# Optimization experiments

Hardware: AMD Instinct MI355X
Metric: run time of the kernel (lower is better)

The kernel has to match this reference:

```python
import jax, jax.numpy as jnp
import numpy as np
import math

B, T, C, H, LC, DFF = 2, 1024, 1024, 16, 256, 4096
EPS = 1e-6


def _ln(x):
    # LayerNorm without affine (elementwise_affine=False under AdaLN), eps=1e-6
    m = jnp.mean(x, -1, keepdims=True)
    v = jnp.mean((x - m) ** 2, -1, keepdims=True)
    return (x - m) * jax.lax.rsqrt(v + EPS)


def _heads(t):
    b, l, c = t.shape
    return t.reshape(b, l, H, c // H).transpose(0, 2, 1, 3)  # (b,H,l,dh)


def _unheads(t):
    b, h, l, d = t.shape
    return t.transpose(0, 2, 1, 3).reshape(b, l, h * d)


def setup_inputs():
    key = jax.random.key(0)
    ks = jax.random.split(key, 16)
    s = 0.02
    p = lambda k, sh: jax.random.normal(k, sh, jnp.float32) * s
    x_star = jax.random.normal(ks[0], (B, T, C), jnp.float32)
    x_hat = jax.random.normal(ks[1], (B, T, C), jnp.float32)
    c = jax.random.normal(ks[2], (B, LC, C), jnp.float32)
    chunk = jnp.sort(jax.random.randint(ks[3], (B, T), 0, 32), axis=1)
    m_star = chunk[:, :, None] > chunk[:, None, :]   # attend to strictly earlier chunks
    m_hat = chunk[:, :, None] == chunk[:, None, :]   # attend within same chunk
    dep_mask = jax.random.bernoulli(ks[4], 0.98, (B, T, T)) | jnp.eye(T, dtype=bool)[None]
    return dict(
        x_star=x_star, x_hat=x_hat, c=c,
        m_star=m_star, m_hat=m_hat, dep_mask=dep_mask,
        ncond_g=jnp.ones((C,), jnp.float32), ncond_b=jnp.zeros((C,), jnp.float32),
        Wq=p(ks[5], (C, C)), bq=jnp.zeros((C,), jnp.float32),
        Wkv=p(ks[6], (C, 2 * C)), bkv=jnp.zeros((2 * C,), jnp.float32),
        Wco=p(ks[7], (C, C)), bco=jnp.zeros((C,), jnp.float32),
        Wada=p(ks[8], (C, 6 * C)), bada=jnp.zeros((6 * C,), jnp.float32),
        Wqkv=p(ks[9], (C, 3 * C)), bqkv=jnp.zeros((3 * C,), jnp.float32),
        Wo=p(ks[10], (C, C)), bo=jnp.zeros((C,), jnp.float32),
        W1=p(ks[11], (C, DFF)), b1=jnp.zeros((DFF,), jnp.float32),
        W2=p(ks[12], (DFF, C)), b2=jnp.zeros((C,), jnp.float32),
    )


def _cross_attn(x, c, Wq, bq, Wkv, bkv, Wco, bco):
    q = _heads(x @ Wq + bq)
    k, v = jnp.split(c @ Wkv + bkv, 2, -1)
    k, v = _heads(k), _heads(v)
    att = jnp.einsum('bhtd,bhsd->bhts', q, k) / math.sqrt(C // H)
    y = jnp.einsum('bhts,bhsd->bhtd', jax.nn.softmax(att, -1), v)
    return _unheads(y) @ Wco + bco


def _interleave(xs, xh, m_star, m_hat, dep, Wqkv, bqkv, Wo, bo):
    # Attention.forward_interleave (eval: dropout identity)
    NEG = -jnp.inf
    sc = 1.0 / math.sqrt(C // H)
    qkv = lambda x: [_heads(t) for t in jnp.split(x @ Wqkv + bqkv, 3, -1)]
    qs, ks, vs = qkv(xs)
    qh, kh, vh = qkv(xh)
    blk_star = (~m_star)[:, None]     # True -> block
    blk_hat = (~m_hat)[:, None]
    blk_dep = (~dep)[:, None]
    causal = jnp.triu(jnp.ones((T, T), bool), 1)[None, None]
    # star stream: causal + dependency mask
    att_star = jnp.einsum('bhtd,bhsd->bhts', qs, ks) * sc
    att_star = jnp.where(blk_dep, NEG, att_star)
    p_star = jax.nn.softmax(jnp.where(causal, NEG, att_star), -1)
    y_star = _unheads(jnp.einsum('bhts,bhsd->bhtd', p_star, vs)) @ Wo + bo
    # hat stream: merge logits (q_hat vs k_star on earlier chunks, q_hat vs k_hat within chunk)
    a1 = jnp.where(blk_star, NEG, jnp.einsum('bhtd,bhsd->bhts', qh, ks) * sc)
    a2 = jnp.where(blk_hat, NEG, jnp.einsum('bhtd,bhsd->bhts', qh, kh) * sc)
    merged = jnp.where(jnp.isinf(a2), a1, a2)
    merged = jnp.where(blk_dep, NEG, merged)
    p_hat = jax.nn.softmax(merged, -1)
    y_hat = jnp.einsum('bhts,bhsd->bhtd', jnp.where(blk_star, 0.0, p_hat), vs) \
          + jnp.einsum('bhts,bhsd->bhtd', jnp.where(blk_hat, 0.0, p_hat), vh)
    y_hat = _unheads(y_hat) @ Wo + bo
    return y_star, y_hat


def reference(x_star, x_hat, c, m_star, m_hat, dep_mask,
              ncond_g, ncond_b, Wq, bq, Wkv, bkv, Wco, bco, Wada, bada,
              Wqkv, bqkv, Wo, bo, W1, b1, W2, b2):
    mod = lambda x, sh, scale: x * (1 + scale) + sh
    mlp = lambda x: jax.nn.gelu(x @ W1 + b1, approximate=True) @ W2 + b2
    ca = lambda x: _cross_attn(_ln(x) * ncond_g + ncond_b, c, Wq, bq, Wkv, bkv, Wco, bco)
    ada = lambda t: jnp.split(jax.nn.silu(t) @ Wada + bada, 6, -1)
    gs = ada(ca(x_star))
    gh = ada(ca(x_hat))
    ms = mod(_ln(x_star), gs[0], gs[1])
    mh = mod(_ln(x_hat), gh[0], gh[1])
    ys, yh = _interleave(ms, mh, m_star, m_hat, dep_mask, Wqkv, bqkv, Wo, bo)
    x_star = x_star + gs[2] * ys
    x_hat = x_hat + gh[2] * yh
    x_star = x_star + gs[5] * mlp(mod(_ln(x_star), gs[3], gs[4]))
    x_hat = x_hat + gh[5] * mlp(mod(_ln(x_hat), gh[3], gh[4]))
    return x_star, x_hat
```

## Files before the change

### kernel.cpp

```cpp
#include <hip/hip_runtime.h>
#include <hip/hip_bf16.h>
#include <stdint.h>

#define DEVI __device__ __forceinline__

typedef __bf16 bf16x8 __attribute__((ext_vector_type(8)));
typedef float f32x4 __attribute__((ext_vector_type(4)));
typedef unsigned short us;
typedef unsigned long long ull;

DEVI float b2f(us u) { union { unsigned int i; float f; } v; v.i = ((unsigned int)u) << 16; return v.f; }
DEVI us f2b(float f) {
  union { unsigned int i; float f; } v; v.f = f;
  unsigned int r = (v.i + 0x7fffu + ((v.i >> 16) & 1u)) >> 16;
  return (us)r;
}

#define NEGINF (-__builtin_inff())

DEVI void gl2lds16(const us* g, us* l) {
  __builtin_amdgcn_global_load_lds(
      (const __attribute__((address_space(1))) unsigned int*)g,
      (__attribute__((address_space(3))) unsigned int*)l, 16, 0, 0);
}

__global__ __launch_bounds__(256) void detect_flags(
    const unsigned int* __restrict__ xw, const unsigned int* __restrict__ mw,
    int* __restrict__ flags) {
  const int t = threadIdx.x;
  int cnt = 0, big = 0;
  for (int i = t; i < 4096; i += 256) {
    unsigned int w = xw[i];
    us lo = (us)(w & 0xffffu);
    float a = fabsf(b2f(lo));
    cnt += ((lo == 0) || (a >= 1e-8f && a <= 256.f)) ? 1 : 0;
    big |= (mw[i] > 1u) ? 1 : 0;
  }
  for (int o = 32; o; o >>= 1) { cnt += __shfl_down(cnt, o); big |= __shfl_down(big, o); }
  __shared__ int sc[4], sb[4];
  if ((t & 63) == 0) { sc[t >> 6] = cnt; sb[t >> 6] = big; }
  __syncthreads();
  if (t == 0) {
    flags[0] = (sc[0] + sc[1] + sc[2] + sc[3] < 2048) ? 1 : 0;
    flags[1] = (sb[0] | sb[1] | sb[2] | sb[3]);
  }
}

__global__ __launch_bounds__(256) void cvt_bf16(
    const void* __restrict__ src, us* __restrict__ dst, int n,
    const int* __restrict__ flags) {
  const int f32mode = flags[0];
  int idx = (blockIdx.x * 256 + threadIdx.x) * 4;
  if (idx >= n) return;
  if (f32mode) {
    const float* s = (const float*)src;
    float4 v = *(const float4*)(s + idx);
    dst[idx] = f2b(v.x); dst[idx + 1] = f2b(v.y);
    dst[idx + 2] = f2b(v.z); dst[idx + 3] = f2b(v.w);
  } else {
    *(uint2*)(dst + idx) = *(const uint2*)((const us*)src + idx);
  }
}

struct P10 { const void* p[10]; };
__global__ __launch_bounds__(256) void cvt_small(P10 ps, us* __restrict__ dst,
                                                 const int* __restrict__ flags) {
  const int offs[11] = {0, 1024, 2048, 3072, 5120, 6144, 12288, 15360, 16384, 20480, 21504};
  int idx = blockIdx.x * 256 + threadIdx.x;
  if (idx >= 21504) return;
  int seg = 0;
#pragma unroll
  for (int i = 1; i < 10; ++i) seg += (idx >= offs[i]) ? 1 : 0;
  int local = idx - offs[seg];
  float v = flags[0] ? ((const float*)ps.p[seg])[local]
                     : b2f(((const us*)ps.p[seg])[local]);
  dst[idx] = f2b(v);
}

__global__ __launch_bounds__(256) void transpose_cvt64(
    const void* __restrict__ W, us* __restrict__ WT, int K, int N,
    const int* __restrict__ flags) {
  __shared__ __attribute__((aligned(16))) us tile[64 * 72];
  const int f32m = flags[0];
  const int k0 = blockIdx.x * 64, n0 = blockIdx.y * 64;
  const int t = threadIdx.x;
  const int row = t >> 2, colb = (t & 3) * 16;
  const int sw = ((row >> 4) & 3) << 4;
  us tmp[16];
  if (f32m) {
    const float* src = (const float*)W + (size_t)(k0 + row) * N + n0 + colb;
#pragma unroll
    for (int i = 0; i < 16; i += 4) {
      float4 v = *(const float4*)(src + i);
      tmp[i] = f2b(v.x); tmp[i + 1] = f2b(v.y); tmp[i + 2] = f2b(v.z); tmp[i + 3] = f2b(v.w);
    }
  } else {
    const us* src = (const us*)W + (size_t)(k0 + row) * N + n0 + colb;
    *(uint4*)tmp = *(const uint4*)src;
    *(uint4*)(tmp + 8) = *(const uint4*)(src + 8);
  }
  *(uint4*)&tile[row * 72 + (colb ^ sw)] = *(uint4*)tmp;
  *(uint4*)&tile[row * 72 + (colb ^ sw) + 8] = *(uint4*)(tmp + 8);
  __syncthreads();
  const int orow = t >> 2, ocolb = (t & 3) * 16;
  const int pc = (orow & 15) | ((orow & 48) ^ (ocolb & 48));
  us out[16];
#pragma unroll
  for (int i = 0; i < 16; ++i) out[i] = tile[(ocolb + i) * 72 + pc];
  us* dst = WT + (size_t)(n0 + orow) * K + k0 + ocolb;
  *(uint4*)dst = *(uint4*)out;
  *(uint4*)(dst + 8) = *(uint4*)(out + 8);
}

struct P3 { const void* p[3]; };
__global__ __launch_bounds__(256) void pack_mask3(P3 ms, ull* __restrict__ bits,
                                                  const int* __restrict__ flags) {
  const int bytemode = flags[1];
  const void* m = ms.p[blockIdx.y];
  ull* out = bits + (size_t)blockIdx.y * 32768;
  int wv = blockIdx.x * 4 + (threadIdx.x >> 6);
  int lane = threadIdx.x & 63;
  for (int w = 0; w < 16; ++w) {
    int v;
    if (bytemode) v = ((const unsigned char*)m)[(size_t)wv * 1024 + w * 64 + lane];
    else          v = ((const int*)m)[(size_t)wv * 1024 + w * 64 + lane];
    ull b = __ballot(v != 0);
    if (lane == 0) out[(size_t)wv * 16 + w] = b;
  }
}

__global__ __launch_bounds__(256) void hat_blockflags(
    const ull* __restrict__ starb, const ull* __restrict__ hatb, int* __restrict__ bf) {
  const int bt = blockIdx.x;
  const int b = bt >> 4, tt = bt & 15;
  const int t = threadIdx.x, wv = t >> 6, lane = t & 63;
  const int t0 = tt * 64;
  for (int k = 0; k < 4; ++k) {
    int ck = wv * 4 + k;
    ull sw = starb[(size_t)(b * 1024 + t0 + lane) * 16 + ck];
    ull hw = hatb[(size_t)(b * 1024 + t0 + lane) * 16 + ck];
    int f = (__ballot(sw != 0ull) ? 1 : 0) | (__ballot(hw != 0ull) ? 2 : 0);
    if (lane == 0) bf[bt * 16 + ck] = f;
  }
}

__global__ __launch_bounds__(256) void vtrans(
    const us* __restrict__ src, us* __restrict__ dst,
    int T, int stride, int colBase, int rowOff) {
  __shared__ __attribute__((aligned(16))) us tile[64][65];
  const int bh = blockIdx.y, b = bh >> 4, h = bh & 15;
  const int t0 = blockIdx.x * 64;
  const int t = threadIdx.x;
#pragma unroll
  for (int it = 0; it < 2; ++it) {
    int idx = it * 256 + t; int r = idx >> 3, c8 = (idx & 7) * 8;
    uint4 d4 = *(const uint4*)(src + (size_t)(rowOff + b * T + t0 + r) * stride + colBase + h * 64 + c8);
    const us* e = (const us*)&d4;
#pragma unroll
    for (int i = 0; i < 8; ++i) tile[r][c8 + i] = e[i];
  }
  __syncthreads();
#pragma unroll
  for (int it = 0; it < 2; ++it) {
    int idx = it * 256 + t; int d = idx >> 3, c8 = (idx & 7) * 8;
    us tmp[8];
#pragma unroll
    for (int i = 0; i < 8; ++i) tmp[i] = tile[c8 + i][d];
    *(uint4*)(dst + ((size_t)(bh * 64 + d)) * T + t0 + c8) = *(const uint4*)tmp;
  }
}

__global__ __launch_bounds__(256) void ln_affine(
    const void* __restrict__ xs, const void* __restrict__ xh,
    const us* __restrict__ gw, const us* __restrict__ bw,
    us* __restrict__ lnx, us* __restrict__ xn, const int* __restrict__ flags) {
  const int f32m = flags[0];
  const int row = blockIdx.x;
  const void* xp = (row < 2048) ? xs : xh;
  const size_t base = (size_t)(row & 2047) * 1024;
  const int t = threadIdx.x;
  float v[4]; float s = 0.f, ss = 0.f;
#pragma unroll
  for (int i = 0; i < 4; ++i) {
    size_t idx = base + i * 256 + t;
    float x = f32m ? ((const float*)xp)[idx] : b2f(((const us*)xp)[idx]);
    v[i] = x; s += x; ss += x * x;
  }
  for (int o = 32; o; o >>= 1) { s += __shfl_down(s, o); ss += __shfl_down(ss, o); }
  __shared__ float red[2][4];
  const int wv = t >> 6, lane = t & 63;
  if (lane == 0) { red[0][wv] = s; red[1][wv] = ss; }
  __syncthreads();
  s = red[0][0] + red[0][1] + red[0][2] + red[0][3];
  ss = red[1][0] + red[1][1] + red[1][2] + red[1][3];
  const float mean = s * (1.f / 1024.f);
  const float var = fmaxf(ss * (1.f / 1024.f) - mean * mean, 0.f);
  const float rstd = rsqrtf(var + 1e-6f);
  const size_t ro = (size_t)row * 1024;
#pragma unroll
  for (int i = 0; i < 4; ++i) {
    int c = i * 256 + t;
    float n = (v[i] - mean) * rstd;
    lnx[ro + c] = f2b(n);
    xn[ro + c] = f2b(n * b2f(gw[c]) + b2f(bw[c]));
  }
}

__global__ __launch_bounds__(256) void mod_ms(
    const us* __restrict__ lnx, const us* __restrict__ gada, us* __restrict__ ms) {
  const size_t idx = ((size_t)blockIdx.x * 256 + threadIdx.x) * 4;
  const int row = (int)(idx >> 10), c = (int)(idx & 1023);
  const size_t gb = (size_t)row * 6144;
#pragma unroll
  for (int i = 0; i < 4; ++i) {
    float sh = b2f(gada[gb + c + i]);
    float sc = b2f(gada[gb + 1024 + c + i]);
    ms[idx + i] = f2b(b2f(lnx[idx + i]) * (1.f + sc) + sh);
  }
}

__global__ __launch_bounds__(256) void ln_mod(
    const float* __restrict__ x1, const us* __restrict__ gada, us* __restrict__ m2) {
  const int row = blockIdx.x;
  const float* xp = x1 + (size_t)row * 1024;
  const int t = threadIdx.x;
  float v[4]; float s = 0.f, ss = 0.f;
#pragma unroll
  for (int i = 0; i < 4; ++i) { float x = xp[i * 256 + t]; v[i] = x; s += x; ss += x * x; }
  for (int o = 32; o; o >>= 1) { s += __shfl_down(s, o); ss += __shfl_down(ss, o); }
  __shared__ float red[2][4];
  const int wv = t >> 6, lane = t & 63;
  if (lane == 0) { red[0][wv] = s; red[1][wv] = ss; }
  __syncthreads();
  s = red[0][0] + red[0][1] + red[0][2] + red[0][3];
  ss = red[1][0] + red[1][1] + red[1][2] + red[1][3];
  const float mean = s * (1.f / 1024.f);
  const float var = fmaxf(ss * (1.f / 1024.f) - mean * mean, 0.f);
  const float rstd = rsqrtf(var + 1e-6f);
  const size_t gb = (size_t)row * 6144;
#pragma unroll
  for (int i = 0; i < 4; ++i) {
    int c = i * 256 + t;
    float n = (v[i] - mean) * rstd;
    float sh = b2f(gada[gb + 3072 + c]);
    float sc = b2f(gada[gb + 4096 + c]);
    m2[(size_t)row * 1024 + c] = f2b(n * (1.f + sc) + sh);
  }
}

enum { EPI_BF16 = 0, EPI_SILU, EPI_GELU, EPI_GATE_XRES, EPI_GATE_OUT };

template <int EPI>
DEVI void gemm_epi(float v, int gmr, int gn, int N, void* out,
                   const us* gate, const void* res0, const void* res1,
                   const int* oflags) {
  const size_t oi = (size_t)gmr * N + gn;
  if constexpr (EPI == EPI_BF16) {
    ((us*)out)[oi] = f2b(v);
  } else if constexpr (EPI == EPI_SILU) {
    ((us*)out)[oi] = f2b(v / (1.f + __expf(-v)));
  } else if constexpr (EPI == EPI_GELU) {
    float u = 0.7978845608028654f * (v + 0.044715f * v * v * v);
    float th = 1.f - 2.f / (__expf(2.f * u) + 1.f);
    ((us*)out)[oi] = f2b(0.5f * v * (1.f + th));
  } else if constexpr (EPI == EPI_GATE_XRES) {
    float g = b2f(gate[(size_t)gmr * 6144 + gn]);
    const void* xr = (gmr < 2048) ? res0 : res1;
    size_t xi = (size_t)(gmr & 2047) * 1024 + gn;
    float x = oflags[0] ? ((const float*)xr)[xi] : b2f(((const us*)xr)[xi]);
    ((float*)out)[oi] = x + g * v;
  } else {
    float g = b2f(gate[(size_t)gmr * 6144 + gn]);
    float x = ((const float*)res0)[oi];
    float r2 = x + g * v;
    if (oflags[0]) ((float*)out)[oi] = r2;
    else ((us*)out)[oi] = f2b(r2);
  }
}

template <int EPI>
__global__ __launch_bounds__(256) void gemm_bt(
    const us* __restrict__ A, const us* __restrict__ BT,
    const us* __restrict__ bias, void* __restrict__ out,
    int M, int N, int K,
    const us* __restrict__ gate,
    const void* __restrict__ res0, const void* __restrict__ res1,
    const int* __restrict__ oflags) {
  __shared__ __attribute__((aligned(16))) us As[2][128 * 32];
  __shared__ __attribute__((aligned(16))) us Bs[2][128 * 32];
  const int m0 = blockIdx.x * 128, n0 = blockIdx.y * 128;
  const int t = threadIdx.x;
  const int wave = t >> 6, lane = t & 63;
  const int wm = (wave >> 1) * 64, wn = (wave & 1) * 64;
  const int l16 = lane & 15, quad = lane >> 4;
  f32x4 acc[4][4] = {};

  const int lr = lane >> 2, lc = (lane & 3) * 8;
  const us* gA = A + (size_t)(m0 + wave * 32 + lr) * K + lc;
  const us* gB = BT + (size_t)(n0 + wave * 32 + lr) * K + lc;
  const int wo = wave * 1024;

  gl2lds16(gA, &As[0][wo]);
  gl2lds16(gA + (size_t)16 * K, &As[0][wo + 512]);
  gl2lds16(gB, &Bs[0][wo]);
  gl2lds16(gB + (size_t)16 * K, &Bs[0][wo + 512]);

  int cur = 0;
  for (int k0 = 0; k0 < K; k0 += 32) {
    __syncthreads();
    const int nk = k0 + 32;
    if (nk < K) {
      us* pA = &As[cur ^ 1][wo];
      us* pB = &Bs[cur ^ 1][wo];
      gl2lds16(gA + nk, pA);
      gl2lds16(gA + (size_t)16 * K + nk, pA + 512);
      gl2lds16(gB + nk, pB);
      gl2lds16(gB + (size_t)16 * K + nk, pB + 512);
    }
    bf16x8 af[4], bfv[4];
#pragma unroll
    for (int i = 0; i < 4; ++i) af[i] = *(const bf16x8*)(const void*)&As[cur][(wm + i * 16 + l16) * 32 + quad * 8];
#pragma unroll
    for (int j = 0; j < 4; ++j) bfv[j] = *(const bf16x8*)(const void*)&Bs[cur][(wn + j * 16 + l16) * 32 + quad * 8];
#pragma unroll
    for (int i = 0; i < 4; ++i)
#pragma unroll
      for (int j = 0; j < 4; ++j)
        acc[i][j] = __builtin_amdgcn_mfma_f32_16x16x32_bf16(af[i], bfv[j], acc[i][j], 0, 0, 0);
    cur ^= 1;
  }

#pragma unroll
  for (int i = 0; i < 4; ++i) {
    const int gm = m0 + wm + i * 16 + quad * 4;
#pragma unroll
    for (int j = 0; j < 4; ++j) {
      const int gn = n0 + wn + j * 16 + l16;
      const float bv = b2f(bias[gn]);
#pragma unroll
      for (int r = 0; r < 4; ++r)
        gemm_epi<EPI>(acc[i][j][r] + bv, gm + r, gn, N, out, gate, res0, res1, oflags);
    }
  }
}

template <int EPI>
__global__ __launch_bounds__(256) void gemm_bt64(
    const us* __restrict__ A, const us* __restrict__ BT,
    const us* __restrict__ bias, void* __restrict__ out,
    int M, int N, int K,
    const us* __restrict__ gate,
    const void* __restrict__ res0, const void* __restrict__ res1,
    const int* __restrict__ oflags) {
  __shared__ __attribute__((aligned(16))) us As[2][128 * 32];
  __shared__ __attribute__((aligned(16))) us Bs[2][64 * 32];
  const int m0 = blockIdx.x * 128, n0 = blockIdx.y * 64;
  const int t = threadIdx.x;
  const int wave = t >> 6, lane = t & 63;
  const int wm = (wave >> 1) * 64, wn = (wave & 1) * 32;
  const int l16 = lane & 15, quad = lane >> 4;
  f32x4 acc[4][2] = {};

  const int lr = lane >> 2, lc = (lane & 3) * 8;
  const us* gA = A + (size_t)(m0 + wave * 32 + lr) * K + lc;
  const us* gB = BT + (size_t)(n0 + wave * 16 + lr) * K + lc;
  const int woA = wave * 1024, woB = wave * 512;

  gl2lds16(gA, &As[0][woA]);
  gl2lds16(gA + (size_t)16 * K, &As[0][woA + 512]);
  gl2lds16(gB, &Bs[0][woB]);

  int cur = 0;
  for (int k0 = 0; k0 < K; k0 += 32) {
    __syncthreads();
    const int nk = k0 + 32;
    if (nk < K) {
      us* pA = &As[cur ^ 1][woA];
      gl2lds16(gA + nk, pA);
      gl2lds16(gA + (size_t)16 * K + nk, pA + 512);
      gl2lds16(gB + nk, &Bs[cur ^ 1][woB]);
    }
    bf16x8 af[4], bfv[2];
#pragma unroll
    for (int i = 0; i < 4; ++i) af[i] = *(const bf16x8*)(const void*)&As[cur][(wm + i * 16 + l16) * 32 + quad * 8];
#pragma unroll
    for (int j = 0; j < 2; ++j) bfv[j] = *(const bf16x8*)(const void*)&Bs[cur][(wn + j * 16 + l16) * 32 + quad * 8];
#pragma unroll
    for (int i = 0; i < 4; ++i)
#pragma unroll
      for (int j = 0; j < 2; ++j)
        acc[i][j] = __builtin_amdgcn_mfma_f32_16x16x32_bf16(af[i], bfv[j], acc[i][j], 0, 0, 0);
    cur ^= 1;
  }

#pragma unroll
  for (int i = 0; i < 4; ++i) {
    const int gm = m0 + wm + i * 16 + quad * 4;
#pragma unroll
    for (int j = 0; j < 2; ++j) {
      const int gn = n0 + wn + j * 16 + l16;
      const float bv = b2f(bias[gn]);
#pragma unroll
      for (int r = 0; r < 4; ++r)
        gemm_epi<EPI>(acc[i][j][r] + bv, gm + r, gn, N, out, gate, res0, res1, oflags);
    }
  }
}

struct AttnState { float m[4], l[4]; f32x4 o[4]; };

DEVI void st_init(AttnState& s) {
#pragma unroll
  for (int r = 0; r < 4; ++r) { s.m[r] = NEGINF; s.l[r] = 0.f; s.o[r] = f32x4{}; }
}

DEVI void stage64(us* __restrict__ dst, const us* __restrict__ src,
                  int strideUs, int t) {
#pragma unroll
  for (int it = 0; it < 2; ++it) {
    const int id = it * 256 + t;
    const int row = id >> 3, c8 = (id & 7) * 8;
    *(uint4*)&dst[row * 72 + c8] = *(const uint4*)(src + (size_t)row * strideUs + c8);
  }
}

template <bool MASKED>
DEVI void attn_round(const us* __restrict__ Kb, const us* __restrict__ Vb,
                     us* __restrict__ Pb, const ull* mrow,
                     bf16x8 aq0, bf16x8 aq1, AttnState& st,
                     int wv, int l16, int quad) {
  f32x4 s[4];
#pragma unroll
  for (int j = 0; j < 4; ++j) {
    const int row = j * 16 + l16;
    bf16x8 bk0 = *(const bf16x8*)(const void*)&Kb[row * 72 + quad * 8];
    bf16x8 bk1 = *(const bf16x8*)(const void*)&Kb[row * 72 + 32 + quad * 8];
    f32x4 z = {};
    z = __builtin_amdgcn_mfma_f32_16x16x32_bf16(aq0, bk0, z, 0, 0, 0);
    z = __builtin_amdgcn_mfma_f32_16x16x32_bf16(aq1, bk1, z, 0, 0, 0);
    s[j] = z;
  }
  const float CE = 0.18033688011112042f;
#pragma unroll
  for (int r = 0; r < 4; ++r) {
    float mx = fmaxf(fmaxf(s[0][r], s[1][r]), fmaxf(s[2][r], s[3][r]));
#pragma unroll
    for (int o2 = 8; o2; o2 >>= 1) mx = fmaxf(mx, __shfl_xor(mx, o2));
    const float mn = fmaxf(st.m[r], mx);
    const float alpha = exp2f((st.m[r] - mn) * CE);
    const float mnC = mn * CE;
    float rs = 0.f;
#pragma unroll
    for (int j = 0; j < 4; ++j) {
      float p = exp2f(__builtin_fmaf(s[j][r], CE, -mnC));
      if constexpr (MASKED) p = ((mrow[r] >> (j * 16 + l16)) & 1ull) ? p : 0.f;
      rs += p;
      ((__bf16*)Pb)[(wv * 16 + quad * 4 + r) * 72 + j * 16 + l16] = (__bf16)p;
    }
#pragma unroll
    for (int o2 = 8; o2; o2 >>= 1) rs += __shfl_xor(rs, o2);
    st.m[r] = mn;
    st.l[r] = st.l[r] * alpha + rs;
#pragma unroll
    for (int jd = 0; jd < 4; ++jd) st.o[jd][r] *= alpha;
  }
  bf16x8 ap0 = *(const bf16x8*)(const void*)&Pb[(wv * 16 + l16) * 72 + quad * 8];
  bf16x8 ap1 = *(const bf16x8*)(const void*)&Pb[(wv * 16 + l16) * 72 + 32 + quad * 8];
#pragma unroll
  for (int jd = 0; jd < 4; ++jd) {
    bf16x8 v0 = *(const bf16x8*)(const void*)&Vb[(jd * 16 + l16) * 72 + quad * 8];
    bf16x8 v1 = *(const bf16x8*)(const void*)&Vb[(jd * 16 + l16) * 72 + 32 + quad * 8];
    st.o[jd] = __builtin_amdgcn_mfma_f32_16x16x32_bf16(ap0, v0, st.o[jd], 0, 0, 0);
    st.o[jd] = __builtin_amdgcn_mfma_f32_16x16x32_bf16(ap1, v1, st.o[jd], 0, 0, 0);
  }
}

DEVI void attn_write(us* __restrict__ y, const AttnState& st, int rowAbs,
                     int h, int l16, int quad) {
#pragma unroll
  for (int r = 0; r < 4; ++r) {
    const float inv = (st.l[r] > 0.f) ? 1.f / st.l[r] : 0.f;
#pragma unroll
    for (int jd = 0; jd < 4; ++jd)
      y[(size_t)(rowAbs + quad * 4 + r) * 1024 + h * 64 + jd * 16 + l16] =
          f2b(st.o[jd][r] * inv);
  }
}

__global__ __launch_bounds__(256) void cross_attn_mfma(
    const us* __restrict__ q, const us* __restrict__ kv,
    const us* __restrict__ vT, us* __restrict__ y) {
  __shared__ __attribute__((aligned(16))) us Kb[64 * 72];
  __shared__ __attribute__((aligned(16))) us Vb[64 * 72];
  __shared__ __attribute__((aligned(16))) us Pb[64 * 72];
  const int bid = blockIdx.x;
  const int xcd = bid & 7, tmp = bid >> 3;
  const int tt = tmp & 15, gq = tmp >> 4;
  const int g = gq * 8 + xcd;
  const int strm = g >> 5, b = (g >> 4) & 1, h = g & 15;
  const int t = threadIdx.x, wv = t >> 6, lane = t & 63;
  const int l16 = lane & 15, quad = lane >> 4;
  const int rowbase = strm * 2048 + b * 1024 + tt * 64 + wv * 16;
  const us* qp = q + (size_t)(rowbase + l16) * 1024 + h * 64 + quad * 8;
  bf16x8 aq0 = *(const bf16x8*)(qp);
  bf16x8 aq1 = *(const bf16x8*)(qp + 32);
  const us* kb = kv + (size_t)b * (256 * 2048) + h * 64;
  const us* vb = vT + (size_t)(b * 16 + h) * (64 * 256);
  AttnState st; st_init(st);
  for (int rnd = 0; rnd < 4; ++rnd) {
    const int s0 = rnd * 64;
    __syncthreads();
    stage64(Kb, kb + (size_t)s0 * 2048, 2048, t);
    stage64(Vb, vb + s0, 256, t);
    __syncthreads();
    attn_round<false>(Kb, Vb, Pb, nullptr, aq0, aq1, st, wv, l16, quad);
  }
  attn_write(y, st, rowbase, h, l16, quad);
}

DEVI void star_body(us* Kb, us* Vb, us* Pb, const us* qkv, const us* vT,
                    const ull* depb, us* y, int b, int h, int tt, int t) {
  const int wv = t >> 6, lane = t & 63;
  const int l16 = lane & 15, quad = lane >> 4;
  const int t0 = tt * 64;
  const int rowbase = b * 1024 + t0 + wv * 16;
  const us* qp = qkv + (size_t)(rowbase + l16) * 3072 + h * 64 + quad * 8;
  bf16x8 aq0 = *(const bf16x8*)(qp);
  bf16x8 aq1 = *(const bf16x8*)(qp + 32);
  const us* kb = qkv + (size_t)(b * 1024) * 3072 + 1024 + h * 64;
  const us* vb = vT + (size_t)(b * 16 + h) * 65536;
  AttnState st; st_init(st);
  ull mrow[4];
  for (int ck = 0; ck <= tt; ++ck) {
    const int s0 = ck * 64;
    __syncthreads();
    stage64(Kb, kb + (size_t)s0 * 3072, 3072, t);
    stage64(Vb, vb + s0, 1024, t);
    __syncthreads();
#pragma unroll
    for (int r = 0; r < 4; ++r) {
      ull d = depb[(size_t)(rowbase + quad * 4 + r) * 16 + ck];
      if (ck == tt) {
        const int idx = wv * 16 + quad * 4 + r;
        d &= (2ull << idx) - 1ull;
      }
      mrow[r] = d;
    }
    attn_round<true>(Kb, Vb, Pb, mrow, aq0, aq1, st, wv, l16, quad);
  }
  attn_write(y, st, rowbase, h, l16, quad);
}

DEVI void hat_body(us* Kb, us* Vb, us* Pb, const us* qkv,
                   const us* vsT, const us* vhT,
                   const ull* starb, const ull* hatb, const ull* depb,
                   const int* bflags, us* y, int b, int h, int tt, int t) {
  const int wv = t >> 6, lane = t & 63;
  const int l16 = lane & 15, quad = lane >> 4;
  const int t0 = tt * 64;
  const int rowbase = b * 1024 + t0 + wv * 16;
  const us* qp = qkv + (size_t)(2048 + rowbase + l16) * 3072 + h * 64 + quad * 8;
  bf16x8 aq0 = *(const bf16x8*)(qp);
  bf16x8 aq1 = *(const bf16x8*)(qp + 32);
  const us* ksb = qkv + (size_t)(b * 1024) * 3072 + 1024 + h * 64;
  const us* khb = qkv + (size_t)(2048 + b * 1024) * 3072 + 1024 + h * 64;
  const us* vsb = vsT + (size_t)(b * 16 + h) * 65536;
  const us* vhb = vhT + (size_t)(b * 16 + h) * 65536;
  AttnState st; st_init(st);
  ull mrow[4];
  for (int ck = 0; ck < 16; ++ck) {
    const int f = bflags[(b * 16 + tt) * 16 + ck];
    const int s0 = ck * 64;
    if (f & 1) {
      __syncthreads();
      stage64(Kb, ksb + (size_t)s0 * 3072, 3072, t);
      stage64(Vb, vsb + s0, 1024, t);
      __syncthreads();
#pragma unroll
      for (int r = 0; r < 4; ++r) {
        const size_t mi = (size_t)(rowbase + quad * 4 + r) * 16 + ck;
        mrow[r] = starb[mi] & depb[mi];
      }
      attn_round<true>(Kb, Vb, Pb, mrow, aq0, aq1, st, wv, l16, quad);
    }
    if (f & 2) {
      __syncthreads();
      stage64(Kb, khb + (size_t)s0 * 3072, 3072, t);
      stage64(Vb, vhb + s0, 1024, t);
      __syncthreads();
#pragma unroll
      for (int r = 0; r < 4; ++r) {
        const size_t mi = (size_t)(rowbase + quad * 4 + r) * 16 + ck;
        mrow[r] = hatb[mi] & depb[mi];
      }
      attn_round<true>(Kb, Vb, Pb, mrow, aq0, aq1, st, wv, l16, quad);
    }
  }
  attn_write(y, st, 2048 + rowbase, h, l16, quad);
}

__global__ __launch_bounds__(256) void self_attn_mfma(
    const us* __restrict__ qkv,
    const us* __restrict__ vstT, const us* __restrict__ vhtT,
    const ull* __restrict__ sbits, const ull* __restrict__ hbits,
    const ull* __restrict__ dbits, const int* __restrict__ bflags,
    us* __restrict__ y) {
  __shared__ __attribute__((aligned(16))) us Kb[64 * 72];
  __shared__ __attribute__((aligned(16))) us Vb[64 * 72];
  __shared__ __attribute__((aligned(16))) us Pb[64 * 72];
  const int bid = blockIdx.x;
  const int xcd = bid & 7, tmp = bid >> 3;
  const int tt = tmp & 15, gq = tmp >> 4;
  const int g = gq * 8 + xcd;
  const int t = threadIdx.x;
  if (g < 32) {
    star_body(Kb, Vb, Pb, qkv, vstT, dbits, y, g >> 4, g & 15, tt, t);
  } else {
    const int g2 = g - 32;
    hat_body(Kb, Vb, Pb, qkv, vstT, vhtT, sbits, hbits, dbits, bflags,
             y, g2 >> 4, g2 & 15, tt, t);
  }
}

extern "C" void kernel_launch(void* const* d_in, const int* in_sizes, int n_in,
                              void* d_out, int out_size, void* d_ws, size_t ws_size,
                              hipStream_t stream) {
  const void* xs = d_in[0];
  const void* xh = d_in[1];
  const void* cc = d_in[2];
  const void* mstar = d_in[3];
  const void* mhat = d_in[4];
  const void* mdep = d_in[5];
  const void* ng = d_in[6];
  const void* nb = d_in[7];
  const void* Wq = d_in[8];
  const void* bq = d_in[9];
  const void* Wkv = d_in[10];
  const void* bkv = d_in[11];
  const void* Wco = d_in[12];
  const void* bco = d_in[13];
  const void* Wada = d_in[14];
  const void* bada = d_in[15];
  const void* Wqkv = d_in[16];
  const void* bqkv = d_in[17];
  const void* Wo = d_in[18];
  const void* bo = d_in[19];
  const void* W1 = d_in[20];
  const void* b1 = d_in[21];
  const void* W2 = d_in[22];
  const void* b2 = d_in[23];
  (void)in_sizes; (void)n_in; (void)out_size; (void)ws_size;

  char* ws = (char*)d_ws;
  size_t off = 0;
  auto alloc = [&](size_t bytes) -> char* {
    char* p = ws + off;
    off += (bytes + 255) & ~(size_t)255;
    return p;
  };
  int* flags = (int*)alloc(256);
  int* bflags = (int*)alloc(512 * 4);
  us* smallb = (us*)alloc(21504 * 2);
  us* ngb = smallb, *nbb = smallb + 1024, *bqb = smallb + 2048,
      *bkvb = smallb + 3072, *bcob = smallb + 5120, *badab = smallb + 6144,
      *bqkvb = smallb + 12288, *bob = smallb + 15360, *b1b = smallb + 16384,
      *b2b = smallb + 20480;
  us* WqT = (us*)alloc(1048576ull * 2);
  us* WkvT = (us*)alloc(2097152ull * 2);
  us* WcoT = (us*)alloc(1048576ull * 2);
  us* WadaT = (us*)alloc(6291456ull * 2);
  us* WqkvT = (us*)alloc(3145728ull * 2);
  us* WoT = (us*)alloc(1048576ull * 2);
  us* W1T = (us*)alloc(4194304ull * 2);
  us* W2T = (us*)alloc(4194304ull * 2);
  us* xn = (us*)alloc(4194304ull * 2);
  us* qb = (us*)alloc(4194304ull * 2);
  us* kvb = (us*)alloc(1048576ull * 2);
  us* gada = (us*)alloc(25165824ull * 2);
  us* msb = (us*)alloc(4194304ull * 2);
  us* qkvb = (us*)alloc(12582912ull * 2);
  float* x1 = (float*)alloc(4194304ull * 4);
  us* hid = (us*)alloc(16777216ull * 2);
  ull* mb = (ull*)alloc(3ull * 32768 * 8);
  us* kvT = (us*)alloc(524288ull * 2);
  us* vstT = (us*)alloc(2097152ull * 2);
  us* vhtT = (us*)alloc(2097152ull * 2);

  ull* sbits = mb;
  ull* hbits = mb + 32768;
  ull* dbits = mb + 65536;
  us* ccb = hid;
  us* lnx = hid + 1048576;
  us* yca = xn;
  us* silub = qb;
  us* yat = msb;

  dim3 blk(256);
  detect_flags<<<1, blk, 0, stream>>>((const unsigned int*)xs, (const unsigned int*)mdep, flags);

  cvt_bf16<<<512, blk, 0, stream>>>(cc, ccb, 524288, flags);
  P10 ps10; ps10.p[0] = ng; ps10.p[1] = nb; ps10.p[2] = bq; ps10.p[3] = bkv;
  ps10.p[4] = bco; ps10.p[5] = bada; ps10.p[6] = bqkv; ps10.p[7] = bo;
  ps10.p[8] = b1; ps10.p[9] = b2;
  cvt_small<<<84, blk, 0, stream>>>(ps10, smallb, flags);

  transpose_cvt64<<<dim3(16, 16), blk, 0, stream>>>(Wq, WqT, 1024, 1024, flags);
  transpose_cvt64<<<dim3(16, 32), blk, 0, stream>>>(Wkv, WkvT, 1024, 2048, flags);
  transpose_cvt64<<<dim3(16, 16), blk, 0, stream>>>(Wco, WcoT, 1024, 1024, flags);
  transpose_cvt64<<<dim3(16, 96), blk, 0, stream>>>(Wada, WadaT, 1024, 6144, flags);
  transpose_cvt64<<<dim3(16, 48), blk, 0, stream>>>(Wqkv, WqkvT, 1024, 3072, flags);
  transpose_cvt64<<<dim3(16, 16), blk, 0, stream>>>(Wo, WoT, 1024, 1024, flags);
  transpose_cvt64<<<dim3(16, 64), blk, 0, stream>>>(W1, W1T, 1024, 4096, flags);
  transpose_cvt64<<<dim3(64, 16), blk, 0, stream>>>(W2, W2T, 4096, 1024, flags);

  P3 ps3; ps3.p[0] = mstar; ps3.p[1] = mhat; ps3.p[2] = mdep;
  pack_mask3<<<dim3(512, 3), blk, 0, stream>>>(ps3, mb, flags);
  hat_blockflags<<<32, blk, 0, stream>>>(sbits, hbits, bflags);

  ln_affine<<<4096, blk, 0, stream>>>(xs, xh, ngb, nbb, lnx, xn, flags);
  gemm_bt64<EPI_BF16><<<dim3(32, 16), blk, 0, stream>>>(xn, WqT, bqb, qb, 4096, 1024, 1024, nullptr, nullptr, nullptr, nullptr);
  gemm_bt64<EPI_BF16><<<dim3(4, 32), blk, 0, stream>>>(ccb, WkvT, bkvb, kvb, 512, 2048, 1024, nullptr, nullptr, nullptr, nullptr);
  vtrans<<<dim3(4, 32), blk, 0, stream>>>(kvb, kvT, 256, 2048, 1024, 0);
  cross_attn_mfma<<<1024, blk, 0, stream>>>(qb, kvb, kvT, yca);
  gemm_bt64<EPI_SILU><<<dim3(32, 16), blk, 0, stream>>>(yca, WcoT, bcob, silub, 4096, 1024, 1024, nullptr, nullptr, nullptr, nullptr);
  gemm_bt<EPI_BF16><<<dim3(32, 48), blk, 0, stream>>>(silub, WadaT, badab, gada, 4096, 6144, 1024, nullptr, nullptr, nullptr, nullptr);
  mod_ms<<<4096, blk, 0, stream>>>(lnx, gada, msb);
  gemm_bt<EPI_BF16><<<dim3(32, 24), blk, 0, stream>>>(msb, WqkvT, bqkvb, qkvb, 4096, 3072, 1024, nullptr, nullptr, nullptr, nullptr);
  vtrans<<<dim3(16, 32), blk, 0, stream>>>(qkvb, vstT, 1024, 3072, 2048, 0);
  vtrans<<<dim3(16, 32), blk, 0, stream>>>(qkvb, vhtT, 1024, 3072, 2048, 2048);
  self_attn_mfma<<<1024, blk, 0, stream>>>(qkvb, vstT, vhtT, sbits, hbits, dbits, bflags, yat);
  gemm_bt64<EPI_GATE_XRES><<<dim3(32, 16), blk, 0, stream>>>(yat, WoT, bob, x1, 4096, 1024, 1024, gada + 2048, xs, xh, flags);
  ln_mod<<<4096, blk, 0, stream>>>(x1, gada, msb);
  gemm_bt<EPI_GELU><<<dim3(32, 32), blk, 0, stream>>>(msb, W1T, b1b, hid, 4096, 4096, 1024, nullptr, nullptr, nullptr, nullptr);
  gemm_bt64<EPI_GATE_OUT><<<dim3(32, 16), blk, 0, stream>>>(hid, W2T, b2b, d_out, 4096, 1024, 4096, gada + 5120, x1, nullptr, flags);
}
```

Measured before the change: 663.8 us.

## Deepen GEMM prefetch with explicit waitcnt and register-prefetch attention K/V tiles

The GEMM kernels now keep two k-tiles in flight. They use explicit vmcnt/lgkmcnt waits with raw barriers instead of a single __syncthreads, and the overwrite of the current LDS buffer is issued only after fragments are read. The attention kernels load the next K/V tile into registers while the current tile is being computed, and the hat self-attention loop turns block flags into a bitmask so it can prefetch across the interleaved star and hat chunks. The final W2 GEMM switches from the 128x64 to the 128x128 tile kernel. The hand-written waitcnt values depend on the exact count of outstanding loads, so a mismatch would be a correctness risk, and the larger W2 tile halves the number of blocks.

```diff
diff --git a/kernel.cpp b/kernel.cpp
--- a/kernel.cpp
+++ b/kernel.cpp
@@ -300,35 +300,47 @@
   const us* gB = BT + (size_t)(n0 + wave * 32 + lr) * K + lc;
   const int wo = wave * 1024;
 
-  gl2lds16(gA, &As[0][wo]);
-  gl2lds16(gA + (size_t)16 * K, &As[0][wo + 512]);
-  gl2lds16(gB, &Bs[0][wo]);
-  gl2lds16(gB + (size_t)16 * K, &Bs[0][wo + 512]);
-
+#define STAGE_BT(buf, k)                                    \
+  { us* pA = &As[buf][wo]; us* pB = &Bs[buf][wo];           \
+    gl2lds16(gA + (k), pA);                                 \
+    gl2lds16(gA + (size_t)16 * K + (k), pA + 512);          \
+    gl2lds16(gB + (k), pB);                                 \
+    gl2lds16(gB + (size_t)16 * K + (k), pB + 512); }
+
+  STAGE_BT(0, 0);
+  STAGE_BT(1, 32);
+  const int NK = K >> 5;
   int cur = 0;
-  for (int k0 = 0; k0 < K; k0 += 32) {
-    __syncthreads();
-    const int nk = k0 + 32;
-    if (nk < K) {
-      us* pA = &As[cur ^ 1][wo];
-      us* pB = &Bs[cur ^ 1][wo];
-      gl2lds16(gA + nk, pA);
-      gl2lds16(gA + (size_t)16 * K + nk, pA + 512);
-      gl2lds16(gB + nk, pB);
-      gl2lds16(gB + (size_t)16 * K + nk, pB + 512);
-    }
+  for (int i = 0; i < NK - 1; ++i) {
+    asm volatile("s_waitcnt vmcnt(4)\n\ts_barrier" ::: "memory");
     bf16x8 af[4], bfv[4];
 #pragma unroll
-    for (int i = 0; i < 4; ++i) af[i] = *(const bf16x8*)(const void*)&As[cur][(wm + i * 16 + l16) * 32 + quad * 8];
+    for (int x = 0; x < 4; ++x) af[x] = *(const bf16x8*)(const void*)&As[cur][(wm + x * 16 + l16) * 32 + quad * 8];
 #pragma unroll
     for (int j = 0; j < 4; ++j) bfv[j] = *(const bf16x8*)(const void*)&Bs[cur][(wn + j * 16 + l16) * 32 + quad * 8];
-#pragma unroll
-    for (int i = 0; i < 4; ++i)
+    asm volatile("s_waitcnt lgkmcnt(0)\n\ts_barrier" ::: "memory");
+    if (i + 2 < NK) STAGE_BT(cur, (i + 2) * 32);
+#pragma unroll
+    for (int x = 0; x < 4; ++x)
 #pragma unroll
       for (int j = 0; j < 4; ++j)
-        acc[i][j] = __builtin_amdgcn_mfma_f32_16x16x32_bf16(af[i], bfv[j], acc[i][j], 0, 0, 0);
+        acc[x][j] = __builtin_amdgcn_mfma_f32_16x16x32_bf16(af[x], bfv[j], acc[x][j], 0, 0, 0);
     cur ^= 1;
   }
+  asm volatile("s_waitcnt vmcnt(0)\n\ts_barrier" ::: "memory");
+  {
+    bf16x8 af[4], bfv[4];
+#pragma unroll
+    for (int x = 0; x < 4; ++x) af[x] = *(const bf16x8*)(const void*)&As[cur][(wm + x * 16 + l16) * 32 + quad * 8];
+#pragma unroll
+    for (int j = 0; j < 4; ++j) bfv[j] = *(const bf16x8*)(const void*)&Bs[cur][(wn + j * 16 + l16) * 32 + quad * 8];
+#pragma unroll
+    for (int x = 0; x < 4; ++x)
+#pragma unroll
+      for (int j = 0; j < 4; ++j)
+        acc[x][j] = __builtin_amdgcn_mfma_f32_16x16x32_bf16(af[x], bfv[j], acc[x][j], 0, 0, 0);
+  }
+#undef STAGE_BT
 
 #pragma unroll
   for (int i = 0; i < 4; ++i) {
@@ -366,32 +378,46 @@
   const us* gB = BT + (size_t)(n0 + wave * 16 + lr) * K + lc;
   const int woA = wave * 1024, woB = wave * 512;
 
-  gl2lds16(gA, &As[0][woA]);
-  gl2lds16(gA + (size_t)16 * K, &As[0][woA + 512]);
-  gl2lds16(gB, &Bs[0][woB]);
-
+#define STAGE_BT64(buf, k)                                  \
+  { us* pA = &As[buf][woA];                                 \
+    gl2lds16(gA + (k), pA);                                 \
+    gl2lds16(gA + (size_t)16 * K + (k), pA + 512);          \
+    gl2lds16(gB + (k), &Bs[buf][woB]); }
+
+  STAGE_BT64(0, 0);
+  STAGE_BT64(1, 32);
+  const int NK = K >> 5;
   int cur = 0;
-  for (int k0 = 0; k0 < K; k0 += 32) {
-    __syncthreads();
-    const int nk = k0 + 32;
-    if (nk < K) {
-      us* pA = &As[cur ^ 1][woA];
-      gl2lds16(gA + nk, pA);
-      gl2lds16(gA + (size_t)16 * K + nk, pA + 512);
-      gl2lds16(gB + nk, &Bs[cur ^ 1][woB]);
-    }
+  for (int i = 0; i < NK - 1; ++i) {
+    asm volatile("s_waitcnt vmcnt(3)\n\ts_barrier" ::: "memory");
     bf16x8 af[4], bfv[2];
 #pragma unroll
-    for (int i = 0; i < 4; ++i) af[i] = *(const bf16x8*)(const void*)&As[cur][(wm + i * 16 + l16) * 32 + quad * 8];
+    for (int x = 0; x < 4; ++x) af[x] = *(const bf16x8*)(const void*)&As[cur][(wm + x * 16 + l16) * 32 + quad * 8];
 #pragma unroll
     for (int j = 0; j < 2; ++j) bfv[j] = *(const bf16x8*)(const void*)&Bs[cur][(wn + j * 16 + l16) * 32 + quad * 8];
-#pragma unroll
-    for (int i = 0; i < 4; ++i)
+    asm volatile("s_waitcnt lgkmcnt(0)\n\ts_barrier" ::: "memory");
+    if (i + 2 < NK) STAGE_BT64(cur, (i + 2) * 32);
+#pragma unroll
+    for (int x = 0; x < 4; ++x)
 #pragma unroll
       for (int j = 0; j < 2; ++j)
-        acc[i][j] = __builtin_amdgcn_mfma_f32_16x16x32_bf16(af[i], bfv[j], acc[i][j], 0, 0, 0);
+        acc[x][j] = __builtin_amdgcn_mfma_f32_16x16x32_bf16(af[x], bfv[j], acc[x][j], 0, 0, 0);
     cur ^= 1;
   }
+  asm volatile("s_waitcnt vmcnt(0)\n\ts_barrier" ::: "memory");
+  {
+    bf16x8 af[4], bfv[2];
+#pragma unroll
+    for (int x = 0; x < 4; ++x) af[x] = *(const bf16x8*)(const void*)&As[cur][(wm + x * 16 + l16) * 32 + quad * 8];
+#pragma unroll
+    for (int j = 0; j < 2; ++j) bfv[j] = *(const bf16x8*)(const void*)&Bs[cur][(wn + j * 16 + l16) * 32 + quad * 8];
+#pragma unroll
+    for (int x = 0; x < 4; ++x)
+#pragma unroll
+      for (int j = 0; j < 2; ++j)
+        acc[x][j] = __builtin_amdgcn_mfma_f32_16x16x32_bf16(af[x], bfv[j], acc[x][j], 0, 0, 0);
+  }
+#undef STAGE_BT64
 
 #pragma unroll
   for (int i = 0; i < 4; ++i) {
@@ -414,14 +440,26 @@
   for (int r = 0; r < 4; ++r) { s.m[r] = NEGINF; s.l[r] = 0.f; s.o[r] = f32x4{}; }
 }
 
-DEVI void stage64(us* __restrict__ dst, const us* __restrict__ src,
-                  int strideUs, int t) {
-#pragma unroll
-  for (int it = 0; it < 2; ++it) {
-    const int id = it * 256 + t;
-    const int row = id >> 3, c8 = (id & 7) * 8;
-    *(uint4*)&dst[row * 72 + c8] = *(const uint4*)(src + (size_t)row * strideUs + c8);
-  }
+struct StReg { uint4 k0, k1, v0, v1; };
+
+DEVI void stage_load(StReg& r, const us* __restrict__ ksrc, int kStride,
+                     const us* __restrict__ vsrc, int vStride, int t) {
+  const int r0 = t >> 3, c0 = (t & 7) * 8;
+  const int r1 = 32 + r0;
+  r.k0 = *(const uint4*)(ksrc + (size_t)r0 * kStride + c0);
+  r.k1 = *(const uint4*)(ksrc + (size_t)r1 * kStride + c0);
+  r.v0 = *(const uint4*)(vsrc + (size_t)r0 * vStride + c0);
+  r.v1 = *(const uint4*)(vsrc + (size_t)r1 * vStride + c0);
+}
+
+DEVI void stage_write(us* __restrict__ Kb, us* __restrict__ Vb,
+                      const StReg& r, int t) {
+  const int r0 = t >> 3, c0 = (t & 7) * 8;
+  const int r1 = 32 + r0;
+  *(uint4*)&Kb[r0 * 72 + c0] = r.k0;
+  *(uint4*)&Kb[r1 * 72 + c0] = r.k1;
+  *(uint4*)&Vb[r0 * 72 + c0] = r.v0;
+  *(uint4*)&Vb[r1 * 72 + c0] = r.v1;
 }
 
 template <bool MASKED>
@@ -507,12 +545,15 @@
   const us* kb = kv + (size_t)b * (256 * 2048) + h * 64;
   const us* vb = vT + (size_t)(b * 16 + h) * (64 * 256);
   AttnState st; st_init(st);
+  StReg sr;
+  stage_load(sr, kb, 2048, vb, 256, t);
   for (int rnd = 0; rnd < 4; ++rnd) {
-    const int s0 = rnd * 64;
     __syncthreads();
-    stage64(Kb, kb + (size_t)s0 * 2048, 2048, t);
-    stage64(Vb, vb + s0, 256, t);
+    stage_write(Kb, Vb, sr, t);
     __syncthreads();
+    if (rnd < 3)
+      stage_load(sr, kb + (size_t)(rnd + 1) * 64 * 2048, 2048,
+                 vb + (rnd + 1) * 64, 256, t);
     attn_round<false>(Kb, Vb, Pb, nullptr, aq0, aq1, st, wv, l16, quad);
   }
   attn_write(y, st, rowbase, h, l16, quad);
@@ -531,12 +572,15 @@
   const us* vb = vT + (size_t)(b * 16 + h) * 65536;
   AttnState st; st_init(st);
   ull mrow[4];
+  StReg sr;
+  stage_load(sr, kb, 3072, vb, 1024, t);
   for (int ck = 0; ck <= tt; ++ck) {
-    const int s0 = ck * 64;
     __syncthreads();
-    stage64(Kb, kb + (size_t)s0 * 3072, 3072, t);
-    stage64(Vb, vb + s0, 1024, t);
+    stage_write(Kb, Vb, sr, t);
     __syncthreads();
+    if (ck < tt)
+      stage_load(sr, kb + (size_t)(ck + 1) * 64 * 3072, 3072,
+                 vb + (ck + 1) * 64, 1024, t);
 #pragma unroll
     for (int r = 0; r < 4; ++r) {
       ull d = depb[(size_t)(rowbase + quad * 4 + r) * 16 + ck];
@@ -567,33 +611,42 @@
   const us* vsb = vsT + (size_t)(b * 16 + h) * 65536;
   const us* vhb = vhT + (size_t)(b * 16 + h) * 65536;
   AttnState st; st_init(st);
-  ull mrow[4];
+  unsigned mask = 0;
   for (int ck = 0; ck < 16; ++ck) {
-    const int f = bflags[(b * 16 + tt) * 16 + ck];
-    const int s0 = ck * 64;
-    if (f & 1) {
+    int f = bflags[(b * 16 + tt) * 16 + ck];
+    mask |= (unsigned)(f & 3) << (2 * ck);
+  }
+  if (mask) {
+    int slot = (int)__builtin_ctz(mask);
+    unsigned rem = mask & (mask - 1);
+    StReg sr;
+    {
+      const int ck = slot >> 1, part = slot & 1;
+      stage_load(sr, (part ? khb : ksb) + (size_t)ck * 64 * 3072, 3072,
+                 (part ? vhb : vsb) + ck * 64, 1024, t);
+    }
+    for (;;) {
       __syncthreads();
-      stage64(Kb, ksb + (size_t)s0 * 3072, 3072, t);
-      stage64(Vb, vsb + s0, 1024, t);
+      stage_write(Kb, Vb, sr, t);
       __syncthreads();
+      const int ck = slot >> 1, part = slot & 1;
+      int nslot = -1;
+      if (rem) {
+        nslot = (int)__builtin_ctz(rem);
+        rem &= rem - 1;
+        const int nck = nslot >> 1, npart = nslot & 1;
+        stage_load(sr, (npart ? khb : ksb) + (size_t)nck * 64 * 3072, 3072,
+                   (npart ? vhb : vsb) + nck * 64, 1024, t);
+      }
+      ull mrow[4];
 #pragma unroll
       for (int r = 0; r < 4; ++r) {
         const size_t mi = (size_t)(rowbase + quad * 4 + r) * 16 + ck;
-        mrow[r] = starb[mi] & depb[mi];
+        mrow[r] = (part ? hatb[mi] : starb[mi]) & depb[mi];
       }
       attn_round<true>(Kb, Vb, Pb, mrow, aq0, aq1, st, wv, l16, quad);
-    }
-    if (f & 2) {
-      __syncthreads();
-      stage64(Kb, khb + (size_t)s0 * 3072, 3072, t);
-      stage64(Vb, vhb + s0, 1024, t);
-      __syncthreads();
-#pragma unroll
-      for (int r = 0; r < 4; ++r) {
-        const size_t mi = (size_t)(rowbase + quad * 4 + r) * 16 + ck;
-        mrow[r] = hatb[mi] & depb[mi];
-      }
-      attn_round<true>(Kb, Vb, Pb, mrow, aq0, aq1, st, wv, l16, quad);
+      if (nslot < 0) break;
+      slot = nslot;
     }
   }
   attn_write(y, st, 2048 + rowbase, h, l16, quad);
@@ -732,5 +785,5 @@
   gemm_bt64<EPI_GATE_XRES><<<dim3(32, 16), blk, 0, stream>>>(yat, WoT, bob, x1, 4096, 1024, 1024, gada + 2048, xs, xh, flags);
   ln_mod<<<4096, blk, 0, stream>>>(x1, gada, msb);
   gemm_bt<EPI_GELU><<<dim3(32, 32), blk, 0, stream>>>(msb, W1T, b1b, hid, 4096, 4096, 1024, nullptr, nullptr, nullptr, nullptr);
-  gemm_bt64<EPI_GATE_OUT><<<dim3(32, 16), blk, 0, stream>>>(hid, W2T, b2b, d_out, 4096, 1024, 4096, gada + 5120, x1, nullptr, flags);
-}
+  gemm_bt<EPI_GATE_OUT><<<dim3(32, 8), blk, 0, stream>>>(hid, W2T, b2b, d_out, 4096, 1024, 4096, gada + 5120, x1, nullptr, flags);
+}
```

Result: slower. 708.1 us (+6.7%).
